# Performance work log

Hardware: AMD Instinct MI355X
Metric: run time of the kernel (lower is better)

## Reference

```python
import jax, jax.numpy as jnp
import numpy as np

# Dimensions
O, D, F_LSOA = 128, 128, 64      # origins, destinations, LSOA feature dim
T, FE, H = 128, 16, 64           # max seq len, edge_feature_dim, gru_hidden
NH, NO, PH = 128, 64, 128        # node_hidden, node_out, pair_hidden
P = O * D                        # number of O-D pairs


def _mlp3(x, W1, b1, W2, b2, W3, b3):
    # Linear->ReLU->Linear->ReLU->Linear (dropout is identity in eval mode)
    h = jax.nn.relu(x @ W1 + b1)
    h = jax.nn.relu(h @ W2 + b2)
    return h @ W3 + b3


def setup_inputs() -> dict:
    key = jax.random.key(0)
    ks = jax.random.split(key, 32)

    def rn(k, shape, s):
        return jax.random.normal(k, shape, dtype=jnp.float32) * s

    inp = {
        "O_feats": rn(ks[0], (O, F_LSOA), 1.0),
        "D_feats": rn(ks[1], (D, F_LSOA), 1.0),
        "seqs": rn(ks[2], (P, T, FE), 1.0),
        "lengths": jax.random.randint(ks[3], (P,), 1, T + 1, dtype=jnp.int32),
        # enc_O
        "WO1": rn(ks[4], (F_LSOA, NH), 0.05), "bO1": jnp.zeros((NH,), jnp.float32),
        "WO2": rn(ks[5], (NH, NH), 0.05),     "bO2": jnp.zeros((NH,), jnp.float32),
        "WO3": rn(ks[6], (NH, NO), 0.05),     "bO3": jnp.zeros((NO,), jnp.float32),
        # enc_D
        "WD1": rn(ks[7], (F_LSOA, NH), 0.05), "bD1": jnp.zeros((NH,), jnp.float32),
        "WD2": rn(ks[8], (NH, NH), 0.05),     "bD2": jnp.zeros((NH,), jnp.float32),
        "WD3": rn(ks[9], (NH, NO), 0.05),     "bD3": jnp.zeros((NO,), jnp.float32),
        # pair_head: 2*node_out -> pair_hidden -> 1
        "Wp1": rn(ks[10], (2 * NO, PH), 0.05), "bp1": jnp.zeros((PH,), jnp.float32),
        "Wp2": rn(ks[11], (PH, 1), 0.05),      "bp2": jnp.zeros((1,), jnp.float32),
        # GRU (gate order r, z, n as in PyTorch)
        "W_ih": rn(ks[12], (FE, 3 * H), 0.1),  "b_ih": jnp.zeros((3 * H,), jnp.float32),
        "W_hh": rn(ks[13], (H, 3 * H), 0.1),   "b_hh": jnp.zeros((3 * H,), jnp.float32),
        # seq_head
        "Ws": rn(ks[14], (H, 1), 0.1),         "bs": jnp.zeros((1,), jnp.float32),
    }
    return inp


def reference(O_feats, D_feats, seqs, lengths,
              WO1, bO1, WO2, bO2, WO3, bO3,
              WD1, bD1, WD2, bD2, WD3, bD3,
              Wp1, bp1, Wp2, bp2,
              W_ih, W_hh, b_ih, b_hh,
              Ws, bs):
    # Node encoders
    eo = _mlp3(O_feats, WO1, bO1, WO2, bO2, WO3, bO3)   # [O, NO]
    ed = _mlp3(D_feats, WD1, bD1, WD2, bD2, WD3, bD3)   # [D, NO]

    # Pairwise score: concat(eo, ed) -> MLP -> softplus
    pair_in = jnp.concatenate([
        jnp.broadcast_to(eo[:, None, :], (O, D, NO)),
        jnp.broadcast_to(ed[None, :, :], (O, D, NO)),
    ], axis=-1)                                          # [O, D, 2*NO]
    hp = jax.nn.relu(pair_in @ Wp1 + bp1)                # [O, D, PH]
    z_pair = (hp @ Wp2 + bp2)[..., 0]                    # [O, D]
    s_pair = jax.nn.softplus(z_pair)

    # Length-masked GRU over all O*D padded sequences (equiv. to pack_padded)
    xT = jnp.swapaxes(seqs, 0, 1)                        # [T, P, FE]
    h0 = jnp.zeros((P, H), jnp.float32)

    def step(h, inp):
        xt, t = inp
        gx = xt @ W_ih + b_ih                            # [P, 3H]
        gh = h @ W_hh + b_hh                             # [P, 3H]
        xr, xz, xn = jnp.split(gx, 3, axis=-1)
        hr, hz, hn = jnp.split(gh, 3, axis=-1)
        r = jax.nn.sigmoid(xr + hr)
        zg = jax.nn.sigmoid(xz + hz)
        n = jnp.tanh(xn + r * hn)
        h_new = (1.0 - zg) * n + zg * h
        h = jnp.where((t < lengths)[:, None], h_new, h)  # freeze past seq end
        return h, None

    h_last, _ = jax.lax.scan(step, h0, (xT, jnp.arange(T)))  # [P, H]

    p_seq = jax.nn.sigmoid(h_last @ Ws + bs)[:, 0].reshape(O, D)
    return jnp.sum(s_pair * p_seq)
```

## Files before the change

kernel.cpp:

```cpp
#include <hip/hip_runtime.h>
#include <hip/hip_bf16.h>

#define O_N 128
#define D_N 128
#define F_LS 64
#define T_MAX 128
#define FE_N 16
#define H_GRU 64
#define NH 128
#define NO 64
#define PH 128

typedef _Float16 f16;
typedef f16 f16x8 __attribute__((ext_vector_type(8)));
typedef f16 f16x4 __attribute__((ext_vector_type(4)));
typedef float f32x4 __attribute__((ext_vector_type(4)));

__device__ __forceinline__ float fast_sigmoid(float x) {
    return __builtin_amdgcn_rcpf(1.f + __expf(-x));
}
__device__ __forceinline__ float fast_tanh(float x) {
    return 1.f - 2.f * __builtin_amdgcn_rcpf(1.f + __expf(2.f * x));
}

__global__ __launch_bounds__(128) void k_enc(
    const float* __restrict__ O_feats, const float* __restrict__ D_feats,
    const float* __restrict__ WO1, const float* __restrict__ bO1,
    const float* __restrict__ WO2, const float* __restrict__ bO2,
    const float* __restrict__ WO3, const float* __restrict__ bO3,
    const float* __restrict__ WD1, const float* __restrict__ bD1,
    const float* __restrict__ WD2, const float* __restrict__ bD2,
    const float* __restrict__ WD3, const float* __restrict__ bD3,
    const float* __restrict__ Wp1,
    float* __restrict__ PA, float* __restrict__ PB,
    int* __restrict__ hist, float* __restrict__ d_out)
{
    __shared__ float h1[NH];
    __shared__ float h2[NH];
    __shared__ float ev[NO];
    const int b = blockIdx.x;
    const int enc = b >> 7;
    const int row = b & 127;
    const int t = threadIdx.x;
    if (b == 0) {
        if (t == 0) d_out[0] = 0.f;
        for (int i = t; i <= 128; i += 128) hist[i] = 0;
    }

    const float* x  = (enc ? D_feats : O_feats) + row * F_LS;
    const float* W1 = enc ? WD1 : WO1;  const float* b1 = enc ? bD1 : bO1;
    const float* W2 = enc ? WD2 : WO2;  const float* b2 = enc ? bD2 : bO2;
    const float* W3 = enc ? WD3 : WO3;  const float* b3 = enc ? bD3 : bO3;

    float a = b1[t];
    #pragma unroll 8
    for (int k = 0; k < F_LS; ++k) a += x[k] * W1[k * NH + t];
    h1[t] = fmaxf(a, 0.f);
    __syncthreads();

    a = b2[t];
    #pragma unroll 8
    for (int k = 0; k < NH; ++k) a += h1[k] * W2[k * NH + t];
    h2[t] = fmaxf(a, 0.f);
    __syncthreads();

    if (t < NO) {
        a = b3[t];
        #pragma unroll 8
        for (int k = 0; k < NH; ++k) a += h2[k] * W3[k * NO + t];
        ev[t] = a;
    }
    __syncthreads();

    const float* Wp = Wp1 + (enc ? NO * PH : 0);
    a = 0.f;
    #pragma unroll 8
    for (int k = 0; k < NO; ++k) a += ev[k] * Wp[k * PH + t];
    (enc ? PB : PA)[row * PH + t] = a;
}

__global__ __launch_bounds__(128) void k_pair(
    const float* __restrict__ PA, const float* __restrict__ PB,
    const float* __restrict__ bp1, const float* __restrict__ Wp2,
    const float* __restrict__ bp2, const int* __restrict__ lengths,
    float* __restrict__ s_pair, int* __restrict__ hist)
{
    const int i = blockIdx.x;
    const int j = threadIdx.x;
    __shared__ float pa[PH];
    __shared__ float b1s[PH];
    __shared__ float w2s[PH];
    pa[j]  = PA[i * PH + j];
    b1s[j] = bp1[j];
    w2s[j] = Wp2[j];
    __syncthreads();
    const float* pb = PB + j * PH;
    float acc = 0.f;
    #pragma unroll 8
    for (int c = 0; c < PH; ++c)
        acc += w2s[c] * fmaxf(pa[c] + pb[c] + b1s[c], 0.f);
    float z = acc + bp2[0];
    float sp = fmaxf(z, 0.f) + log1pf(__expf(-fabsf(z)));
    s_pair[i * 128 + j] = sp;
    atomicAdd(&hist[lengths[i * 128 + j]], 1);
}

__global__ __launch_bounds__(256) void k_scan(int* __restrict__ hist)
{
    __shared__ int sh[129];
    const int t = threadIdx.x;
    if (t < 129) sh[t] = hist[t];
    __syncthreads();
    if (t == 0) {
        int run = 0;
        for (int i = 0; i <= 128; ++i) { int v = sh[i]; sh[i] = run; run += v; }
    }
    __syncthreads();
    if (t < 129) hist[t] = sh[t];
}

__global__ __launch_bounds__(256) void k_scatter(
    const int* __restrict__ lengths, int* __restrict__ hist, int* __restrict__ perm)
{
    const int i = blockIdx.x * 256 + threadIdx.x;
    const int len = lengths[i];
    const int pos = atomicAdd(&hist[len], 1);
    perm[pos] = i;
}

__global__ __launch_bounds__(256, 4) void k_gru(
    const float* __restrict__ seqs, const int* __restrict__ lengths,
    const int* __restrict__ perm,
    const float* __restrict__ W_ih, const float* __restrict__ b_ih,
    const float* __restrict__ W_hh, const float* __restrict__ b_hh,
    const float* __restrict__ Ws, const float* __restrict__ bs,
    const float* __restrict__ s_pair, float* __restrict__ d_out)
{
    __shared__ __align__(16) f16 hbuf[2 * 16 * 72];
    __shared__ __align__(16) f16 xbuf[2 * 16 * 40];
    __shared__ float red[64];
    const int tid = threadIdx.x;
    const int w  = tid >> 6;
    const int l  = tid & 63;
    const int q  = l >> 4;
    const int n  = l & 15;
    const int c  = w * 16 + n;
    const int pb = blockIdx.x * 16;

    f16x8 wh[3][2], wi[3];
    #pragma unroll
    for (int g = 0; g < 3; ++g) {
        const int gb = g * 64;
        #pragma unroll
        for (int ks = 0; ks < 2; ++ks)
            #pragma unroll
            for (int j = 0; j < 8; ++j)
                wh[g][ks][j] = (f16)W_hh[(ks * 32 + q * 8 + j) * 192 + gb + c];
        #pragma unroll
        for (int j = 0; j < 8; ++j) {
            int k = q * 8 + j;
            wi[g][j] = (k < FE_N) ? (f16)W_ih[k * 192 + gb + c] : (f16)0.f;
        }
    }

    const float brz_r = b_ih[c] + b_hh[c];
    const float brz_z = b_ih[64 + c] + b_hh[64 + c];
    const float bxn   = b_ih[128 + c];
    const float bhn   = b_hh[128 + c];
    const float wsc   = Ws[c];

    int pr[4], len[4];
    #pragma unroll
    for (int r = 0; r < 4; ++r) {
        pr[r]  = perm[pb + q * 4 + r];
        len[r] = lengths[pr[r]];
    }
    int ml = max(max(len[0], len[1]), max(len[2], len[3]));
    ml = max(ml, __shfl_xor(ml, 16));
    ml = max(ml, __shfl_xor(ml, 32));
    const int maxlen = __builtin_amdgcn_readfirstlane(ml);

    {
        f16x8 z8 = {(f16)0, (f16)0, (f16)0, (f16)0, (f16)0, (f16)0, (f16)0, (f16)0};
        if (tid < 144) *(f16x8*)&hbuf[tid * 8] = z8;
        if (tid >= 192) {
            int id = tid - 192;
            int buf = id >> 5;
            int rr = (id & 31) >> 1, ch = id & 1;
            *(f16x8*)&xbuf[buf * 640 + rr * 40 + 16 + ch * 8] = z8;
        }
    }

    const int pl = tid >> 4, ft = tid & 15;
    const int pp = perm[pb + pl];
    const float* xptr = seqs + (size_t)pp * (T_MAX * FE_N) + ft;
    xbuf[pl * 40 + ft] = (f16)xptr[0];
    float xv = xptr[((1 < maxlen) ? 1 : (maxlen - 1)) * 16];

    float hold[4] = {0.f, 0.f, 0.f, 0.f};
    const f32x4 zero4 = {0.f, 0.f, 0.f, 0.f};
    __syncthreads();

    for (int t = 0; t < maxlen; ++t) {
        const f16* hb  = hbuf + (t & 1) * 1152;
        f16*       hbn = hbuf + ((t + 1) & 1) * 1152;
        const f16* xb  = xbuf + (t & 1) * 640;
        f16*       xbn = xbuf + ((t + 1) & 1) * 640;

        f16x8 ah0 = *(const f16x8*)&hb[n * 72 + q * 8];
        f16x8 ah1 = *(const f16x8*)&hb[n * 72 + 32 + q * 8];
        f16x8 ax  = *(const f16x8*)&xb[n * 40 + q * 8];

        xbn[pl * 40 + ft] = (f16)xv;
        int tn = (t + 2 < maxlen) ? (t + 2) : (maxlen - 1);
        xv = xptr[tn * 16];

        f32x4 ar = __builtin_amdgcn_mfma_f32_16x16x32_f16(ah0, wh[0][0], zero4, 0, 0, 0);
        ar = __builtin_amdgcn_mfma_f32_16x16x32_f16(ah1, wh[0][1], ar, 0, 0, 0);
        ar = __builtin_amdgcn_mfma_f32_16x16x32_f16(ax,  wi[0],    ar, 0, 0, 0);
        f32x4 az = __builtin_amdgcn_mfma_f32_16x16x32_f16(ah0, wh[1][0], zero4, 0, 0, 0);
        az = __builtin_amdgcn_mfma_f32_16x16x32_f16(ah1, wh[1][1], az, 0, 0, 0);
        az = __builtin_amdgcn_mfma_f32_16x16x32_f16(ax,  wi[1],    az, 0, 0, 0);
        f32x4 ahn = __builtin_amdgcn_mfma_f32_16x16x32_f16(ah0, wh[2][0], zero4, 0, 0, 0);
        ahn = __builtin_amdgcn_mfma_f32_16x16x32_f16(ah1, wh[2][1], ahn, 0, 0, 0);
        f32x4 axn = __builtin_amdgcn_mfma_f32_16x16x32_f16(ax, wi[2], zero4, 0, 0, 0);

        #pragma unroll
        for (int r = 0; r < 4; ++r) {
            float rg   = fast_sigmoid(ar[r] + brz_r);
            float zg   = fast_sigmoid(az[r] + brz_z);
            float nn   = fast_tanh(fmaf(rg, ahn[r] + bhn, axn[r] + bxn));
            float hnew = fmaf(zg, hold[r] - nn, nn);
            hnew = (t < len[r]) ? hnew : hold[r];
            hold[r] = hnew;
            hbn[(q * 4 + r) * 72 + c] = (f16)hnew;
        }
        __syncthreads();
    }

    float part[4];
    #pragma unroll
    for (int r = 0; r < 4; ++r) part[r] = hold[r] * wsc;
    #pragma unroll
    for (int off = 1; off < 16; off <<= 1)
        #pragma unroll
        for (int r = 0; r < 4; ++r)
            part[r] += __shfl_xor(part[r], off);
    if (n == 0) {
        #pragma unroll
        for (int r = 0; r < 4; ++r) red[w * 16 + q * 4 + r] = part[r];
    }
    __syncthreads();
    if (tid < 16) {
        float s = red[tid] + red[16 + tid] + red[32 + tid] + red[48 + tid];
        float pv = fast_sigmoid(s + bs[0]);
        float contrib = s_pair[perm[pb + tid]] * pv;
        #pragma unroll
        for (int off = 1; off < 16; off <<= 1)
            contrib += __shfl_xor(contrib, off);
        if (tid == 0) atomicAdd(d_out, contrib);
    }
}

extern "C" void kernel_launch(void* const* d_in, const int* in_sizes, int n_in,
                              void* d_out, int out_size, void* d_ws, size_t ws_size,
                              hipStream_t stream)
{
    const float* O_feats = (const float*)d_in[0];
    const float* D_feats = (const float*)d_in[1];
    const float* seqs    = (const float*)d_in[2];
    const int*   lengths = (const int*)d_in[3];
    const float* WO1 = (const float*)d_in[4];  const float* bO1 = (const float*)d_in[5];
    const float* WO2 = (const float*)d_in[6];  const float* bO2 = (const float*)d_in[7];
    const float* WO3 = (const float*)d_in[8];  const float* bO3 = (const float*)d_in[9];
    const float* WD1 = (const float*)d_in[10]; const float* bD1 = (const float*)d_in[11];
    const float* WD2 = (const float*)d_in[12]; const float* bD2 = (const float*)d_in[13];
    const float* WD3 = (const float*)d_in[14]; const float* bD3 = (const float*)d_in[15];
    const float* Wp1 = (const float*)d_in[16]; const float* bp1 = (const float*)d_in[17];
    const float* Wp2 = (const float*)d_in[18]; const float* bp2 = (const float*)d_in[19];
    const float* W_ih = (const float*)d_in[20]; const float* b_ih = (const float*)d_in[21];
    const float* W_hh = (const float*)d_in[22]; const float* b_hh = (const float*)d_in[23];
    const float* Ws   = (const float*)d_in[24]; const float* bs   = (const float*)d_in[25];

    float* out    = (float*)d_out;
    float* PA     = (float*)d_ws;
    float* PB     = PA + 128 * 128;
    float* s_pair = PB + 128 * 128;
    int*   hist   = (int*)(s_pair + 16384);
    int*   perm   = hist + 256;

    k_enc<<<256, 128, 0, stream>>>(O_feats, D_feats,
                                   WO1, bO1, WO2, bO2, WO3, bO3,
                                   WD1, bD1, WD2, bD2, WD3, bD3,
                                   Wp1, PA, PB, hist, out);
    k_pair<<<128, 128, 0, stream>>>(PA, PB, bp1, Wp2, bp2, lengths, s_pair, hist);
    k_scan<<<1, 256, 0, stream>>>(hist);
    k_scatter<<<64, 256, 0, stream>>>(lengths, hist, perm);
    k_gru<<<1024, 256, 0, stream>>>(seqs, lengths, perm, W_ih, b_ih, W_hh, b_hh,
                                    Ws, bs, s_pair, out);
}
```

Measured before the change: 381.1 us.

## Pair long and short GRU groups per block, sort descending in one kernel

Replaces the histogram, scan and scatter kernels with a single-block counting sort that orders pairs by descending length. The GRU kernel now launches 512 blocks, and each one processes group g and then group NG-1-g, so long and short sequences are paired to balance work across blocks. The per-step input staging through shared memory is removed: each lane loads its x row directly as float4 and prefetches one step ahead into registers. The launch-bounds occupancy hint drops to 2, and the MFMA order is changed so the input products come first. The risks are fewer resident blocks to hide latency, the long serial GRU chain inside each block, and the single-block sort sitting on the critical path.

```diff
diff --git a/kernel.cpp b/kernel.cpp
--- a/kernel.cpp
+++ b/kernel.cpp
@@ -10,6 +10,7 @@
 #define NH 128
 #define NO 64
 #define PH 128
+#define NG 1024
 
 typedef _Float16 f16;
 typedef f16 f16x8 __attribute__((ext_vector_type(8)));
@@ -32,8 +33,7 @@
     const float* __restrict__ WD2, const float* __restrict__ bD2,
     const float* __restrict__ WD3, const float* __restrict__ bD3,
     const float* __restrict__ Wp1,
-    float* __restrict__ PA, float* __restrict__ PB,
-    int* __restrict__ hist, float* __restrict__ d_out)
+    float* __restrict__ PA, float* __restrict__ PB, float* __restrict__ d_out)
 {
     __shared__ float h1[NH];
     __shared__ float h2[NH];
@@ -42,10 +42,7 @@
     const int enc = b >> 7;
     const int row = b & 127;
     const int t = threadIdx.x;
-    if (b == 0) {
-        if (t == 0) d_out[0] = 0.f;
-        for (int i = t; i <= 128; i += 128) hist[i] = 0;
-    }
+    if (b == 0 && t == 0) d_out[0] = 0.f;
 
     const float* x  = (enc ? D_feats : O_feats) + row * F_LS;
     const float* W1 = enc ? WD1 : WO1;  const float* b1 = enc ? bD1 : bO1;
@@ -82,8 +79,7 @@
 __global__ __launch_bounds__(128) void k_pair(
     const float* __restrict__ PA, const float* __restrict__ PB,
     const float* __restrict__ bp1, const float* __restrict__ Wp2,
-    const float* __restrict__ bp2, const int* __restrict__ lengths,
-    float* __restrict__ s_pair, int* __restrict__ hist)
+    const float* __restrict__ bp2, float* __restrict__ s_pair)
 {
     const int i = blockIdx.x;
     const int j = threadIdx.x;
@@ -102,33 +98,36 @@
     float z = acc + bp2[0];
     float sp = fmaxf(z, 0.f) + log1pf(__expf(-fabsf(z)));
     s_pair[i * 128 + j] = sp;
-    atomicAdd(&hist[lengths[i * 128 + j]], 1);
-}
-
-__global__ __launch_bounds__(256) void k_scan(int* __restrict__ hist)
-{
-    __shared__ int sh[129];
+}
+
+__global__ __launch_bounds__(1024) void k_sort(
+    const int* __restrict__ lengths, int* __restrict__ perm)
+{
+    __shared__ int cnt[130];
+    __shared__ int suf[130];
     const int t = threadIdx.x;
-    if (t < 129) sh[t] = hist[t];
-    __syncthreads();
-    if (t == 0) {
-        int run = 0;
-        for (int i = 0; i <= 128; ++i) { int v = sh[i]; sh[i] = run; run += v; }
-    }
-    __syncthreads();
-    if (t < 129) hist[t] = sh[t];
-}
-
-__global__ __launch_bounds__(256) void k_scatter(
-    const int* __restrict__ lengths, int* __restrict__ hist, int* __restrict__ perm)
-{
-    const int i = blockIdx.x * 256 + threadIdx.x;
-    const int len = lengths[i];
-    const int pos = atomicAdd(&hist[len], 1);
-    perm[pos] = i;
-}
-
-__global__ __launch_bounds__(256, 4) void k_gru(
+    if (t < 130) cnt[t] = 0;
+    __syncthreads();
+    for (int i = t; i < 16384; i += 1024) atomicAdd(&cnt[lengths[i]], 1);
+    __syncthreads();
+    if (t < 130) suf[t] = cnt[t];
+    __syncthreads();
+    for (int d = 1; d < 130; d <<= 1) {
+        int v = 0;
+        if (t < 130) { v = suf[t]; if (t + d < 130) v += suf[t + d]; }
+        __syncthreads();
+        if (t < 130) suf[t] = v;
+        __syncthreads();
+    }
+    if (t < 129) cnt[t] = (t + 1 < 130) ? suf[t + 1] : 0;
+    __syncthreads();
+    for (int i = t; i < 16384; i += 1024) {
+        int pos = atomicAdd(&cnt[lengths[i]], 1);
+        perm[pos] = i;
+    }
+}
+
+__global__ __launch_bounds__(256, 2) void k_gru(
     const float* __restrict__ seqs, const int* __restrict__ lengths,
     const int* __restrict__ perm,
     const float* __restrict__ W_ih, const float* __restrict__ b_ih,
@@ -137,7 +136,6 @@
     const float* __restrict__ s_pair, float* __restrict__ d_out)
 {
     __shared__ __align__(16) f16 hbuf[2 * 16 * 72];
-    __shared__ __align__(16) f16 xbuf[2 * 16 * 40];
     __shared__ float red[64];
     const int tid = threadIdx.x;
     const int w  = tid >> 6;
@@ -145,7 +143,8 @@
     const int q  = l >> 4;
     const int n  = l & 15;
     const int c  = w * 16 + n;
-    const int pb = blockIdx.x * 16;
+    const f32x4 zero4 = {0.f, 0.f, 0.f, 0.f};
+    const f16x8 zero8 = {(f16)0, (f16)0, (f16)0, (f16)0, (f16)0, (f16)0, (f16)0, (f16)0};
 
     f16x8 wh[3][2], wi[3];
     #pragma unroll
@@ -162,103 +161,98 @@
             wi[g][j] = (k < FE_N) ? (f16)W_ih[k * 192 + gb + c] : (f16)0.f;
         }
     }
-
     const float brz_r = b_ih[c] + b_hh[c];
     const float brz_z = b_ih[64 + c] + b_hh[64 + c];
     const float bxn   = b_ih[128 + c];
     const float bhn   = b_hh[128 + c];
     const float wsc   = Ws[c];
-
-    int pr[4], len[4];
-    #pragma unroll
-    for (int r = 0; r < 4; ++r) {
-        pr[r]  = perm[pb + q * 4 + r];
-        len[r] = lengths[pr[r]];
-    }
-    int ml = max(max(len[0], len[1]), max(len[2], len[3]));
-    ml = max(ml, __shfl_xor(ml, 16));
-    ml = max(ml, __shfl_xor(ml, 32));
-    const int maxlen = __builtin_amdgcn_readfirstlane(ml);
-
-    {
-        f16x8 z8 = {(f16)0, (f16)0, (f16)0, (f16)0, (f16)0, (f16)0, (f16)0, (f16)0};
-        if (tid < 144) *(f16x8*)&hbuf[tid * 8] = z8;
-        if (tid >= 192) {
-            int id = tid - 192;
-            int buf = id >> 5;
-            int rr = (id & 31) >> 1, ch = id & 1;
-            *(f16x8*)&xbuf[buf * 640 + rr * 40 + 16 + ch * 8] = z8;
-        }
-    }
-
-    const int pl = tid >> 4, ft = tid & 15;
-    const int pp = perm[pb + pl];
-    const float* xptr = seqs + (size_t)pp * (T_MAX * FE_N) + ft;
-    xbuf[pl * 40 + ft] = (f16)xptr[0];
-    float xv = xptr[((1 < maxlen) ? 1 : (maxlen - 1)) * 16];
-
-    float hold[4] = {0.f, 0.f, 0.f, 0.f};
-    const f32x4 zero4 = {0.f, 0.f, 0.f, 0.f};
-    __syncthreads();
-
-    for (int t = 0; t < maxlen; ++t) {
-        const f16* hb  = hbuf + (t & 1) * 1152;
-        f16*       hbn = hbuf + ((t + 1) & 1) * 1152;
-        const f16* xb  = xbuf + (t & 1) * 640;
-        f16*       xbn = xbuf + ((t + 1) & 1) * 640;
-
-        f16x8 ah0 = *(const f16x8*)&hb[n * 72 + q * 8];
-        f16x8 ah1 = *(const f16x8*)&hb[n * 72 + 32 + q * 8];
-        f16x8 ax  = *(const f16x8*)&xb[n * 40 + q * 8];
-
-        xbn[pl * 40 + ft] = (f16)xv;
-        int tn = (t + 2 < maxlen) ? (t + 2) : (maxlen - 1);
-        xv = xptr[tn * 16];
-
-        f32x4 ar = __builtin_amdgcn_mfma_f32_16x16x32_f16(ah0, wh[0][0], zero4, 0, 0, 0);
-        ar = __builtin_amdgcn_mfma_f32_16x16x32_f16(ah1, wh[0][1], ar, 0, 0, 0);
-        ar = __builtin_amdgcn_mfma_f32_16x16x32_f16(ax,  wi[0],    ar, 0, 0, 0);
-        f32x4 az = __builtin_amdgcn_mfma_f32_16x16x32_f16(ah0, wh[1][0], zero4, 0, 0, 0);
-        az = __builtin_amdgcn_mfma_f32_16x16x32_f16(ah1, wh[1][1], az, 0, 0, 0);
-        az = __builtin_amdgcn_mfma_f32_16x16x32_f16(ax,  wi[1],    az, 0, 0, 0);
-        f32x4 ahn = __builtin_amdgcn_mfma_f32_16x16x32_f16(ah0, wh[2][0], zero4, 0, 0, 0);
-        ahn = __builtin_amdgcn_mfma_f32_16x16x32_f16(ah1, wh[2][1], ahn, 0, 0, 0);
-        f32x4 axn = __builtin_amdgcn_mfma_f32_16x16x32_f16(ax, wi[2], zero4, 0, 0, 0);
-
+    const float bsv   = bs[0];
+
+    for (int gi = 0; gi < 2; ++gi) {
+        const int g  = gi ? (NG - 1 - (int)blockIdx.x) : (int)blockIdx.x;
+        const int pb = g * 16;
+
+        int pr[4], len[4];
         #pragma unroll
         for (int r = 0; r < 4; ++r) {
-            float rg   = fast_sigmoid(ar[r] + brz_r);
-            float zg   = fast_sigmoid(az[r] + brz_z);
-            float nn   = fast_tanh(fmaf(rg, ahn[r] + bhn, axn[r] + bxn));
-            float hnew = fmaf(zg, hold[r] - nn, nn);
-            hnew = (t < len[r]) ? hnew : hold[r];
-            hold[r] = hnew;
-            hbn[(q * 4 + r) * 72 + c] = (f16)hnew;
-        }
-        __syncthreads();
-    }
-
-    float part[4];
-    #pragma unroll
-    for (int r = 0; r < 4; ++r) part[r] = hold[r] * wsc;
-    #pragma unroll
-    for (int off = 1; off < 16; off <<= 1)
-        #pragma unroll
-        for (int r = 0; r < 4; ++r)
-            part[r] += __shfl_xor(part[r], off);
-    if (n == 0) {
-        #pragma unroll
-        for (int r = 0; r < 4; ++r) red[w * 16 + q * 4 + r] = part[r];
-    }
-    __syncthreads();
-    if (tid < 16) {
-        float s = red[tid] + red[16 + tid] + red[32 + tid] + red[48 + tid];
-        float pv = fast_sigmoid(s + bs[0]);
-        float contrib = s_pair[perm[pb + tid]] * pv;
+            pr[r]  = perm[pb + q * 4 + r];
+            len[r] = lengths[pr[r]];
+        }
+        int ml = max(max(len[0], len[1]), max(len[2], len[3]));
+        ml = max(ml, __shfl_xor(ml, 16));
+        ml = max(ml, __shfl_xor(ml, 32));
+        const int maxlen = __builtin_amdgcn_readfirstlane(ml);
+
+        if (tid < 144) *(f16x8*)&hbuf[tid * 8] = zero8;
+
+        const int pp = perm[pb + n];
+        const float4* xp = (const float4*)(seqs + (size_t)pp * (T_MAX * FE_N)) + q * 2;
+        float4 xa = {0.f, 0.f, 0.f, 0.f}, xb = xa;
+        if (q < 2) { xa = xp[0]; xb = xp[1]; }
+
+        float hold[4] = {0.f, 0.f, 0.f, 0.f};
+        __syncthreads();
+
+        for (int t = 0; t < maxlen; ++t) {
+            f16x8 ax = zero8;
+            if (q < 2) {
+                ax[0] = (f16)xa.x; ax[1] = (f16)xa.y; ax[2] = (f16)xa.z; ax[3] = (f16)xa.w;
+                ax[4] = (f16)xb.x; ax[5] = (f16)xb.y; ax[6] = (f16)xb.z; ax[7] = (f16)xb.w;
+                int tn = (t + 1 < maxlen) ? (t + 1) : t;
+                xa = xp[tn * 4];
+                xb = xp[tn * 4 + 1];
+            }
+            const f16* hb  = hbuf + (t & 1) * 1152;
+            f16*       hbn = hbuf + ((t + 1) & 1) * 1152;
+
+            f16x8 ah0 = *(const f16x8*)&hb[n * 72 + q * 8];
+            f16x8 ah1 = *(const f16x8*)&hb[n * 72 + 32 + q * 8];
+
+            f32x4 axn = __builtin_amdgcn_mfma_f32_16x16x32_f16(ax, wi[2], zero4, 0, 0, 0);
+            f32x4 ar  = __builtin_amdgcn_mfma_f32_16x16x32_f16(ax, wi[0], zero4, 0, 0, 0);
+            ar  = __builtin_amdgcn_mfma_f32_16x16x32_f16(ah0, wh[0][0], ar, 0, 0, 0);
+            ar  = __builtin_amdgcn_mfma_f32_16x16x32_f16(ah1, wh[0][1], ar, 0, 0, 0);
+            f32x4 az  = __builtin_amdgcn_mfma_f32_16x16x32_f16(ax, wi[1], zero4, 0, 0, 0);
+            az  = __builtin_amdgcn_mfma_f32_16x16x32_f16(ah0, wh[1][0], az, 0, 0, 0);
+            az  = __builtin_amdgcn_mfma_f32_16x16x32_f16(ah1, wh[1][1], az, 0, 0, 0);
+            f32x4 ahn = __builtin_amdgcn_mfma_f32_16x16x32_f16(ah0, wh[2][0], zero4, 0, 0, 0);
+            ahn = __builtin_amdgcn_mfma_f32_16x16x32_f16(ah1, wh[2][1], ahn, 0, 0, 0);
+
+            #pragma unroll
+            for (int r = 0; r < 4; ++r) {
+                float rg   = fast_sigmoid(ar[r] + brz_r);
+                float zg   = fast_sigmoid(az[r] + brz_z);
+                float nn   = fast_tanh(fmaf(rg, ahn[r] + bhn, axn[r] + bxn));
+                float hnew = fmaf(zg, hold[r] - nn, nn);
+                hnew = (t < len[r]) ? hnew : hold[r];
+                hold[r] = hnew;
+                hbn[(q * 4 + r) * 72 + c] = (f16)hnew;
+            }
+            __syncthreads();
+        }
+
+        float part[4];
+        #pragma unroll
+        for (int r = 0; r < 4; ++r) part[r] = hold[r] * wsc;
         #pragma unroll
         for (int off = 1; off < 16; off <<= 1)
-            contrib += __shfl_xor(contrib, off);
-        if (tid == 0) atomicAdd(d_out, contrib);
+            #pragma unroll
+            for (int r = 0; r < 4; ++r)
+                part[r] += __shfl_xor(part[r], off);
+        if (n == 0) {
+            #pragma unroll
+            for (int r = 0; r < 4; ++r) red[w * 16 + q * 4 + r] = part[r];
+        }
+        __syncthreads();
+        if (tid < 16) {
+            float s = red[tid] + red[16 + tid] + red[32 + tid] + red[48 + tid];
+            float pv = fast_sigmoid(s + bsv);
+            float contrib = s_pair[perm[pb + tid]] * pv;
+            #pragma unroll
+            for (int off = 1; off < 16; off <<= 1)
+                contrib += __shfl_xor(contrib, off);
+            if (tid == 0) atomicAdd(d_out, contrib);
+        }
     }
 }
 
@@ -286,16 +280,14 @@
     float* PA     = (float*)d_ws;
     float* PB     = PA + 128 * 128;
     float* s_pair = PB + 128 * 128;
-    int*   hist   = (int*)(s_pair + 16384);
-    int*   perm   = hist + 256;
+    int*   perm   = (int*)(s_pair + 16384);
 
     k_enc<<<256, 128, 0, stream>>>(O_feats, D_feats,
                                    WO1, bO1, WO2, bO2, WO3, bO3,
                                    WD1, bD1, WD2, bD2, WD3, bD3,
-                                   Wp1, PA, PB, hist, out);
-    k_pair<<<128, 128, 0, stream>>>(PA, PB, bp1, Wp2, bp2, lengths, s_pair, hist);
-    k_scan<<<1, 256, 0, stream>>>(hist);
-    k_scatter<<<64, 256, 0, stream>>>(lengths, hist, perm);
-    k_gru<<<1024, 256, 0, stream>>>(seqs, lengths, perm, W_ih, b_ih, W_hh, b_hh,
-                                    Ws, bs, s_pair, out);
-}
+                                   Wp1, PA, PB, out);
+    k_pair<<<128, 128, 0, stream>>>(PA, PB, bp1, Wp2, bp2, s_pair);
+    k_sort<<<1, 1024, 0, stream>>>(lengths, perm);
+    k_gru<<<512, 256, 0, stream>>>(seqs, lengths, perm, W_ih, b_ih, W_hh, b_hh,
+                                   Ws, bs, s_pair, out);
+}
```

Result: slower. 391.6 us (+2.8%).
